# Kernel optimization log

Measured on AMD Instinct MI355X. Metric: run time of the kernel, lower is better.

## Reference

```python
import jax, jax.numpy as jnp
import numpy as np

NUM_Q = 500000
NUM_E = 250000
DIM = 256
HEADS = 4
NEG_SLOPE = 0.01
EPS = 1e-16


def setup_inputs() -> dict:
    key = jax.random.key(0)
    k1, k2, k3, k4, k5 = jax.random.split(key, 5)
    x_q = jax.random.normal(k1, (NUM_Q, DIM), dtype=jnp.float32)
    x_edge = jax.random.normal(k2, (NUM_E, DIM), dtype=jnp.float32)
    edge_ids = jax.random.randint(k3, (NUM_Q,), 0, NUM_E, dtype=jnp.int64)
    # learned params: w_q (input_dim, output_dim), attention weight (H, 2*dim/H)
    w_q = jax.random.normal(k4, (DIM, DIM), dtype=jnp.float32) / np.sqrt(DIM)
    weight = jax.random.normal(k5, (HEADS, 2 * DIM // HEADS), dtype=jnp.float32) / np.sqrt(2 * DIM // HEADS)
    return {"x_q": x_q, "x_edge": x_edge, "w_q": w_q, "weight": weight, "edge_ids": edge_ids}


def reference(x_q, x_edge, w_q, weight, edge_ids):
    nq = x_q.shape[0]
    ne = x_edge.shape[0]
    h = weight.shape[0]
    # project qualifier pairs: (nq, dim) -> (nq, H, d_head)
    xq = (x_q @ w_q).reshape(nq, h, -1)
    # gather edge reps per qualifier pair: (nq, H, d_head)
    xe = x_edge[edge_ids].reshape(nq, h, -1)
    # per-head attention logits: eh
    alpha = jnp.einsum('ehd,hd->eh', jnp.concatenate([xe, xq], axis=-1), weight)
    alpha = jax.nn.leaky_relu(alpha, NEG_SLOPE)
    # segment softmax grouped by edge_ids (numerically stable)
    seg_max = jax.ops.segment_max(alpha, edge_ids, num_segments=ne)
    seg_max = jnp.where(jnp.isfinite(seg_max), seg_max, 0.0)  # empty segments
    ex = jnp.exp(alpha - seg_max[edge_ids])
    seg_sum = jax.ops.segment_sum(ex, edge_ids, num_segments=ne)
    alpha = ex / (seg_sum[edge_ids] + EPS)
    # weight qualifier reps and scatter-add to edges
    xq = (alpha[..., None] * xq).reshape(nq, -1)
    return jax.ops.segment_sum(xq, edge_ids, num_segments=ne)
```

## Files before the change

### kernel.cpp

```cpp
#include <hip/hip_runtime.h>
#include <hip/hip_bf16.h>

#define DIM 256
#define HEADS 4
#define NEG_SLOPE 0.01f

typedef unsigned short u16;
typedef __attribute__((ext_vector_type(8))) short short8;
typedef __attribute__((ext_vector_type(4))) float f32x4;
typedef __attribute__((ext_vector_type(4))) unsigned short u16x4;

__device__ __forceinline__ u16 f2bf(float f) {
    unsigned u = __float_as_uint(f);
    unsigned r = (u + 0x7fffu + ((u >> 16) & 1u)) >> 16;
    return (u16)r;
}
__device__ __forceinline__ float bf2f(u16 h) {
    return __uint_as_float(((unsigned)h) << 16);
}
__device__ __forceinline__ void split2(float f0, float f1, unsigned& hi, unsigned& lo) {
    unsigned u0 = __float_as_uint(f0), u1 = __float_as_uint(f1);
    hi = (u0 >> 16) | (u1 & 0xffff0000u);
    float r0 = f0 - __uint_as_float(u0 & 0xffff0000u);
    float r1 = f1 - __uint_as_float(u1 & 0xffff0000u);
    lo = (__float_as_uint(r0) >> 16) | (__float_as_uint(r1) & 0xffff0000u);
}

__global__ __launch_bounds__(256) void prepb_kernel(const float* __restrict__ B,
                                                    u16* __restrict__ BThi) {
    int k = blockIdx.x;
    int n = threadIdx.x;
    BThi[n * 256 + k] = f2bf(B[k * 256 + n]);
}

__global__ __launch_bounds__(256) void beta_kernel(const float* __restrict__ xe,
                                                   const float* __restrict__ weight,
                                                   float* __restrict__ beta, int NE) {
    int wid = blockIdx.x * 4 + (threadIdx.x >> 6);
    if (wid >= NE) return;
    int lane = threadIdx.x & 63;
    int h = lane >> 4;
    float4 v = *reinterpret_cast<const float4*>(xe + (size_t)wid * DIM + lane * 4);
    float4 w = *reinterpret_cast<const float4*>(weight + h * 128 + (lane & 15) * 4);
    float p = v.x * w.x + v.y * w.y + v.z * w.z + v.w * w.w;
    p += __shfl_xor(p, 1);
    p += __shfl_xor(p, 2);
    p += __shfl_xor(p, 4);
    p += __shfl_xor(p, 8);
    if ((lane & 15) == 0) beta[(size_t)wid * 4 + h] = p;
}

__global__ __launch_bounds__(256, 3) void gemm_gamma_kernel(const float* __restrict__ A,
                                                            const u16* __restrict__ BThi,
                                                            const float* __restrict__ weight,
                                                            u16* __restrict__ xq_out,
                                                            float* __restrict__ gamma, int NQ) {
    __shared__ u16 Ahi_s[64 * 32];
    __shared__ u16 Alo_s[64 * 32];
    __shared__ u16 Bhi_s[256 * 32];

    const int t = threadIdx.x;
    const int lane = t & 63;
    const int wc = t >> 6;
    const int lr = lane & 15;
    const int kg = lane >> 4;
    const long brow = (long)blockIdx.x * 64;

    f32x4 acc[4][4];
#pragma unroll
    for (int m = 0; m < 4; ++m)
#pragma unroll
        for (int n = 0; n < 4; ++n) acc[m][n] = (f32x4){0.f, 0.f, 0.f, 0.f};

    for (int k0 = 0; k0 < DIM; k0 += 32) {
#pragma unroll
        for (int i = 0; i < 2; ++i) {
            int slot = t + i * 256;
            int row = slot >> 3, c4 = slot & 7;
            long grow = brow + row;
            if (grow >= NQ) grow = NQ - 1;
            float4 v = *reinterpret_cast<const float4*>(A + grow * DIM + k0 + c4 * 4);
            unsigned h01, l01, h23, l23;
            split2(v.x, v.y, h01, l01);
            split2(v.z, v.w, h23, l23);
            int swz = (c4 >> 1) ^ (row & 3) ^ ((row >> 2) & 3);
            int off = row * 32 + (swz << 3) + ((c4 & 1) << 2);
            *reinterpret_cast<uint2*>(&Ahi_s[off]) = make_uint2(h01, h23);
            *reinterpret_cast<uint2*>(&Alo_s[off]) = make_uint2(l01, l23);
        }
#pragma unroll
        for (int i = 0; i < 4; ++i) {
            int slot = t + i * 256;
            int n = slot >> 2, c = slot & 3;
            uint4 vh = *reinterpret_cast<const uint4*>(BThi + n * 256 + k0 + c * 8);
            int swz = c ^ (n & 3) ^ ((n >> 2) & 3);
            *reinterpret_cast<uint4*>(&Bhi_s[n * 32 + (swz << 3)]) = vh;
        }
        __syncthreads();

        short8 bh[4];
#pragma unroll
        for (int n = 0; n < 4; ++n) {
            int nn = wc * 64 + n * 16 + lr;
            int off = nn * 32 + ((kg ^ (nn & 3) ^ ((nn >> 2) & 3)) << 3);
            bh[n] = *reinterpret_cast<const short8*>(&Bhi_s[off]);
        }
#pragma unroll
        for (int m = 0; m < 4; ++m) {
            int rr = m * 16 + lr;
            int off = rr * 32 + ((kg ^ (rr & 3) ^ ((rr >> 2) & 3)) << 3);
            short8 ah = *reinterpret_cast<const short8*>(&Ahi_s[off]);
            short8 al = *reinterpret_cast<const short8*>(&Alo_s[off]);
#pragma unroll
            for (int n = 0; n < 4; ++n) {
                acc[m][n] = __builtin_amdgcn_mfma_f32_16x16x32_bf16(ah, bh[n], acc[m][n], 0, 0, 0);
                acc[m][n] = __builtin_amdgcn_mfma_f32_16x16x32_bf16(al, bh[n], acc[m][n], 0, 0, 0);
            }
        }
        __syncthreads();
    }

    float wv[4];
#pragma unroll
    for (int n = 0; n < 4; ++n) wv[n] = weight[wc * 128 + 64 + n * 16 + lr];

#pragma unroll
    for (int m = 0; m < 4; ++m) {
#pragma unroll
        for (int r = 0; r < 4; ++r) {
            long row = brow + m * 16 + kg * 4 + r;
            bool ok = row < NQ;
            float p = 0.f;
#pragma unroll
            for (int n = 0; n < 4; ++n) {
                float v = acc[m][n][r];
                if (ok) xq_out[row * DIM + wc * 64 + n * 16 + lr] = f2bf(v);
                p = fmaf(v, wv[n], p);
            }
            p += __shfl_xor(p, 1);
            p += __shfl_xor(p, 2);
            p += __shfl_xor(p, 4);
            p += __shfl_xor(p, 8);
            if (ok && lr == 0) gamma[row * 4 + wc] = p;
        }
    }
}

__global__ __launch_bounds__(256) void logits_ex_kernel(const float* __restrict__ beta,
                                                        const float* __restrict__ gamma,
                                                        const int* __restrict__ eids,
                                                        float* __restrict__ exv,
                                                        float* __restrict__ segsum,
                                                        unsigned* __restrict__ counts, int NQ) {
    int e = blockIdx.x * blockDim.x + threadIdx.x;
    if (e >= NQ) return;
    int j = eids[e];
    float4 g = *reinterpret_cast<const float4*>(gamma + (size_t)e * 4);
    float4 b = *reinterpret_cast<const float4*>(beta + (size_t)j * 4);
    float l[4] = {b.x + g.x, b.y + g.y, b.z + g.z, b.w + g.w};
    float ex[4];
#pragma unroll
    for (int h = 0; h < 4; ++h) {
        l[h] = l[h] > 0.f ? l[h] : NEG_SLOPE * l[h];
        ex[h] = __expf(l[h]);
    }
    *reinterpret_cast<float4*>(exv + (size_t)e * 4) = make_float4(ex[0], ex[1], ex[2], ex[3]);
#pragma unroll
    for (int h = 0; h < 4; ++h) atomicAdd(&segsum[(size_t)j * 4 + h], ex[h]);
    atomicAdd(&counts[j], 1u);
}

__global__ __launch_bounds__(256) void scan1_kernel(const unsigned* __restrict__ counts,
                                                    unsigned* __restrict__ offs,
                                                    unsigned* __restrict__ blocksums, int NE) {
    __shared__ unsigned s[256];
    int t = threadIdx.x;
    int base = blockIdx.x * 1024 + t * 4;
    unsigned v[4], sum = 0;
#pragma unroll
    for (int i = 0; i < 4; ++i) {
        v[i] = (base + i < NE) ? counts[base + i] : 0u;
        sum += v[i];
    }
    s[t] = sum;
    __syncthreads();
    for (int off = 1; off < 256; off <<= 1) {
        unsigned y = (t >= off) ? s[t - off] : 0u;
        __syncthreads();
        s[t] += y;
        __syncthreads();
    }
    unsigned excl = s[t] - sum;
#pragma unroll
    for (int i = 0; i < 4; ++i) {
        if (base + i < NE) offs[base + i] = excl;
        excl += v[i];
    }
    if (t == 255) blocksums[blockIdx.x] = s[255];
}

__global__ __launch_bounds__(256) void scan2_kernel(unsigned* __restrict__ blocksums, int NB) {
    __shared__ unsigned s[256];
    int t = threadIdx.x;
    unsigned v = (t < NB) ? blocksums[t] : 0u;
    s[t] = v;
    __syncthreads();
    for (int off = 1; off < 256; off <<= 1) {
        unsigned y = (t >= off) ? s[t - off] : 0u;
        __syncthreads();
        s[t] += y;
        __syncthreads();
    }
    if (t < NB) blocksums[t] = s[t] - v;
}

__global__ __launch_bounds__(256) void scan3_kernel(unsigned* __restrict__ offs,
                                                    const unsigned* __restrict__ blocksums,
                                                    unsigned* __restrict__ cursor, int NE) {
    int t = threadIdx.x;
    int base = blockIdx.x * 1024 + t * 4;
    unsigned add = blocksums[blockIdx.x];
#pragma unroll
    for (int i = 0; i < 4; ++i) {
        if (base + i < NE) {
            unsigned o = offs[base + i] + add;
            offs[base + i] = o;
            cursor[base + i] = o;
        }
    }
}

__global__ __launch_bounds__(256) void fill_kernel(const int* __restrict__ eids,
                                                   unsigned* __restrict__ cursor,
                                                   int* __restrict__ qlist, int NQ) {
    int e = blockIdx.x * blockDim.x + threadIdx.x;
    if (e >= NQ) return;
    int j = eids[e];
    unsigned pos = atomicAdd(&cursor[j], 1u);
    qlist[pos] = e;
}

__global__ __launch_bounds__(256) void gather_kernel(const float* __restrict__ exv,
                                                     const float* __restrict__ segsum,
                                                     const unsigned* __restrict__ offs,
                                                     const unsigned* __restrict__ counts,
                                                     const int* __restrict__ qlist,
                                                     const u16* __restrict__ xq,
                                                     float* __restrict__ out, int NE) {
    int j = blockIdx.x * 4 + (threadIdx.x >> 6);
    if (j >= NE) return;
    int lane = threadIdx.x & 63;
    int h = lane >> 4;
    unsigned beg = offs[j];
    unsigned n = counts[j];
    float inv = 1.0f / (segsum[(size_t)j * 4 + h] + 1e-16f);
    float4 a0 = make_float4(0.f, 0.f, 0.f, 0.f);
    float4 a1 = make_float4(0.f, 0.f, 0.f, 0.f);
    unsigned i = 0;
    for (; i + 2 <= n; i += 2) {
        int q0 = qlist[beg + i];
        int q1 = qlist[beg + i + 1];
        float w0 = exv[(size_t)q0 * 4 + h] * inv;
        float w1 = exv[(size_t)q1 * 4 + h] * inv;
        u16x4 v0 = *reinterpret_cast<const u16x4*>(xq + (size_t)q0 * DIM + lane * 4);
        u16x4 v1 = *reinterpret_cast<const u16x4*>(xq + (size_t)q1 * DIM + lane * 4);
        a0.x = fmaf(w0, bf2f(v0.x), a0.x); a1.x = fmaf(w1, bf2f(v1.x), a1.x);
        a0.y = fmaf(w0, bf2f(v0.y), a0.y); a1.y = fmaf(w1, bf2f(v1.y), a1.y);
        a0.z = fmaf(w0, bf2f(v0.z), a0.z); a1.z = fmaf(w1, bf2f(v1.z), a1.z);
        a0.w = fmaf(w0, bf2f(v0.w), a0.w); a1.w = fmaf(w1, bf2f(v1.w), a1.w);
    }
    if (i < n) {
        int q0 = qlist[beg + i];
        float w0 = exv[(size_t)q0 * 4 + h] * inv;
        u16x4 v0 = *reinterpret_cast<const u16x4*>(xq + (size_t)q0 * DIM + lane * 4);
        a0.x = fmaf(w0, bf2f(v0.x), a0.x);
        a0.y = fmaf(w0, bf2f(v0.y), a0.y);
        a0.z = fmaf(w0, bf2f(v0.z), a0.z);
        a0.w = fmaf(w0, bf2f(v0.w), a0.w);
    }
    float4 acc = make_float4(a0.x + a1.x, a0.y + a1.y, a0.z + a1.z, a0.w + a1.w);
    *reinterpret_cast<float4*>(out + (size_t)j * DIM + lane * 4) = acc;
}

extern "C" void kernel_launch(void* const* d_in, const int* in_sizes, int n_in,
                              void* d_out, int out_size, void* d_ws, size_t ws_size,
                              hipStream_t stream) {
    (void)n_in; (void)out_size; (void)ws_size;
    const float* x_q    = (const float*)d_in[0];
    const float* x_edge = (const float*)d_in[1];
    const float* w_q    = (const float*)d_in[2];
    const float* weight = (const float*)d_in[3];
    const int*   eids   = (const int*)d_in[4];
    const int NQ = in_sizes[0] / DIM;
    const int NE = in_sizes[1] / DIM;
    float* out = (float*)d_out;

    u16*      xq        = (u16*)d_ws;
    float*    gamma     = (float*)(xq + (size_t)NQ * DIM);
    float*    exv       = gamma + (size_t)NQ * 4;
    float*    beta      = exv + (size_t)NQ * 4;
    float*    segsum    = beta + (size_t)NE * 4;
    unsigned* counts    = (unsigned*)(segsum + (size_t)NE * 4);
    unsigned* offs      = counts + NE;
    unsigned* cursor    = offs + NE;
    int*      qlist     = (int*)(cursor + NE);
    unsigned* blocksums = (unsigned*)(qlist + NQ);
    u16*      BThi      = (u16*)(blocksums + 256);

    const int NB = (NE + 1023) / 1024;

    hipMemsetAsync(segsum, 0, (size_t)NE * 4 * sizeof(float), stream);
    hipMemsetAsync(counts, 0, (size_t)NE * sizeof(unsigned), stream);

    prepb_kernel<<<256, 256, 0, stream>>>(w_q, BThi);
    beta_kernel<<<(NE + 3) / 4, 256, 0, stream>>>(x_edge, weight, beta, NE);
    gemm_gamma_kernel<<<(NQ + 63) / 64, 256, 0, stream>>>(x_q, BThi, weight, xq, gamma, NQ);
    logits_ex_kernel<<<(NQ + 255) / 256, 256, 0, stream>>>(beta, gamma, eids, exv, segsum, counts, NQ);
    scan1_kernel<<<NB, 256, 0, stream>>>(counts, offs, blocksums, NE);
    scan2_kernel<<<1, 256, 0, stream>>>(blocksums, NB);
    scan3_kernel<<<NB, 256, 0, stream>>>(offs, blocksums, cursor, NE);
    fill_kernel<<<(NQ + 255) / 256, 256, 0, stream>>>(eids, cursor, qlist, NQ);
    gather_kernel<<<(NE + 3) / 4, 256, 0, stream>>>(exv, segsum, offs, counts, qlist, xq, out, NE);
}
```

Before: 581.7 us.

## Fuse logits/exp/atomics into GEMM epilogue and drop bf16 split-precision A

Moves the leaky-relu, exp, segment-sum atomics and count atomics into the GEMM epilogue, removing the gamma buffer and the separate logits kernel launch. The A operand is now rounded to a single bf16 instead of a hi/lo bf16 pair, which halves the MFMA count and A shared-memory traffic. The exchange is lower precision in the projection and logits.

```diff
diff --git a/kernel.cpp b/kernel.cpp
--- a/kernel.cpp
+++ b/kernel.cpp
@@ -17,13 +17,6 @@
 }
 __device__ __forceinline__ float bf2f(u16 h) {
     return __uint_as_float(((unsigned)h) << 16);
-}
-__device__ __forceinline__ void split2(float f0, float f1, unsigned& hi, unsigned& lo) {
-    unsigned u0 = __float_as_uint(f0), u1 = __float_as_uint(f1);
-    hi = (u0 >> 16) | (u1 & 0xffff0000u);
-    float r0 = f0 - __uint_as_float(u0 & 0xffff0000u);
-    float r1 = f1 - __uint_as_float(u1 & 0xffff0000u);
-    lo = (__float_as_uint(r0) >> 16) | (__float_as_uint(r1) & 0xffff0000u);
 }
 
 __global__ __launch_bounds__(256) void prepb_kernel(const float* __restrict__ B,
@@ -50,13 +43,17 @@
     if ((lane & 15) == 0) beta[(size_t)wid * 4 + h] = p;
 }
 
-__global__ __launch_bounds__(256, 3) void gemm_gamma_kernel(const float* __restrict__ A,
+__global__ __launch_bounds__(256, 3) void gemm_fused_kernel(const float* __restrict__ A,
                                                             const u16* __restrict__ BThi,
                                                             const float* __restrict__ weight,
+                                                            const float* __restrict__ beta,
+                                                            const int* __restrict__ eids,
                                                             u16* __restrict__ xq_out,
-                                                            float* __restrict__ gamma, int NQ) {
+                                                            float* __restrict__ exv,
+                                                            float* __restrict__ segsum,
+                                                            unsigned* __restrict__ counts,
+                                                            int NQ) {
     __shared__ u16 Ahi_s[64 * 32];
-    __shared__ u16 Alo_s[64 * 32];
     __shared__ u16 Bhi_s[256 * 32];
 
     const int t = threadIdx.x;
@@ -80,13 +77,11 @@
             long grow = brow + row;
             if (grow >= NQ) grow = NQ - 1;
             float4 v = *reinterpret_cast<const float4*>(A + grow * DIM + k0 + c4 * 4);
-            unsigned h01, l01, h23, l23;
-            split2(v.x, v.y, h01, l01);
-            split2(v.z, v.w, h23, l23);
+            u16x4 hv;
+            hv.x = f2bf(v.x); hv.y = f2bf(v.y); hv.z = f2bf(v.z); hv.w = f2bf(v.w);
             int swz = (c4 >> 1) ^ (row & 3) ^ ((row >> 2) & 3);
             int off = row * 32 + (swz << 3) + ((c4 & 1) << 2);
-            *reinterpret_cast<uint2*>(&Ahi_s[off]) = make_uint2(h01, h23);
-            *reinterpret_cast<uint2*>(&Alo_s[off]) = make_uint2(l01, l23);
+            *reinterpret_cast<u16x4*>(&Ahi_s[off]) = hv;
         }
 #pragma unroll
         for (int i = 0; i < 4; ++i) {
@@ -110,12 +105,9 @@
             int rr = m * 16 + lr;
             int off = rr * 32 + ((kg ^ (rr & 3) ^ ((rr >> 2) & 3)) << 3);
             short8 ah = *reinterpret_cast<const short8*>(&Ahi_s[off]);
-            short8 al = *reinterpret_cast<const short8*>(&Alo_s[off]);
-#pragma unroll
-            for (int n = 0; n < 4; ++n) {
+#pragma unroll
+            for (int n = 0; n < 4; ++n)
                 acc[m][n] = __builtin_amdgcn_mfma_f32_16x16x32_bf16(ah, bh[n], acc[m][n], 0, 0, 0);
-                acc[m][n] = __builtin_amdgcn_mfma_f32_16x16x32_bf16(al, bh[n], acc[m][n], 0, 0, 0);
-            }
         }
         __syncthreads();
     }
@@ -141,33 +133,17 @@
             p += __shfl_xor(p, 2);
             p += __shfl_xor(p, 4);
             p += __shfl_xor(p, 8);
-            if (ok && lr == 0) gamma[row * 4 + wc] = p;
-        }
-    }
-}
-
-__global__ __launch_bounds__(256) void logits_ex_kernel(const float* __restrict__ beta,
-                                                        const float* __restrict__ gamma,
-                                                        const int* __restrict__ eids,
-                                                        float* __restrict__ exv,
-                                                        float* __restrict__ segsum,
-                                                        unsigned* __restrict__ counts, int NQ) {
-    int e = blockIdx.x * blockDim.x + threadIdx.x;
-    if (e >= NQ) return;
-    int j = eids[e];
-    float4 g = *reinterpret_cast<const float4*>(gamma + (size_t)e * 4);
-    float4 b = *reinterpret_cast<const float4*>(beta + (size_t)j * 4);
-    float l[4] = {b.x + g.x, b.y + g.y, b.z + g.z, b.w + g.w};
-    float ex[4];
-#pragma unroll
-    for (int h = 0; h < 4; ++h) {
-        l[h] = l[h] > 0.f ? l[h] : NEG_SLOPE * l[h];
-        ex[h] = __expf(l[h]);
-    }
-    *reinterpret_cast<float4*>(exv + (size_t)e * 4) = make_float4(ex[0], ex[1], ex[2], ex[3]);
-#pragma unroll
-    for (int h = 0; h < 4; ++h) atomicAdd(&segsum[(size_t)j * 4 + h], ex[h]);
-    atomicAdd(&counts[j], 1u);
+            if (ok && lr == 0) {
+                int j = eids[row];
+                float l = beta[(size_t)j * 4 + wc] + p;
+                l = l > 0.f ? l : NEG_SLOPE * l;
+                float e = __expf(l);
+                exv[row * 4 + wc] = e;
+                atomicAdd(&segsum[(size_t)j * 4 + wc], e);
+                if (wc == 0) atomicAdd(&counts[j], 1u);
+            }
+        }
+    }
 }
 
 __global__ __launch_bounds__(256) void scan1_kernel(const unsigned* __restrict__ counts,
@@ -296,8 +272,7 @@
     float* out = (float*)d_out;
 
     u16*      xq        = (u16*)d_ws;
-    float*    gamma     = (float*)(xq + (size_t)NQ * DIM);
-    float*    exv       = gamma + (size_t)NQ * 4;
+    float*    exv       = (float*)(xq + (size_t)NQ * DIM);
     float*    beta      = exv + (size_t)NQ * 4;
     float*    segsum    = beta + (size_t)NE * 4;
     unsigned* counts    = (unsigned*)(segsum + (size_t)NE * 4);
@@ -314,8 +289,8 @@
 
     prepb_kernel<<<256, 256, 0, stream>>>(w_q, BThi);
     beta_kernel<<<(NE + 3) / 4, 256, 0, stream>>>(x_edge, weight, beta, NE);
-    gemm_gamma_kernel<<<(NQ + 63) / 64, 256, 0, stream>>>(x_q, BThi, weight, xq, gamma, NQ);
-    logits_ex_kernel<<<(NQ + 255) / 256, 256, 0, stream>>>(beta, gamma, eids, exv, segsum, counts, NQ);
+    gemm_fused_kernel<<<(NQ + 63) / 64, 256, 0, stream>>>(x_q, BThi, weight, beta, eids,
+                                                          xq, exv, segsum, counts, NQ);
     scan1_kernel<<<NB, 256, 0, stream>>>(counts, offs, blocksums, NE);
     scan2_kernel<<<1, 256, 0, stream>>>(blocksums, NB);
     scan3_kernel<<<NB, 256, 0, stream>>>(offs, blocksums, cursor, NE);
```

Measured after the change: 562.7 us. -3.3%, faster.
